# Kernel tuning notes

Hardware: AMD Instinct MI355X
Metric: run time of the kernel (lower is better)

Reference implementation:

```python
import jax, jax.numpy as jnp
import numpy as np

B, N, DIM, HEADS = 4, 2048, 512, 8
LN_EPS = 1e-5


def setup_inputs() -> dict:
    key = jax.random.key(0)
    ks = jax.random.split(key, 16)
    w = lambda k: jax.random.normal(k, (DIM, DIM), jnp.float32) * 0.02
    bv = lambda k: jax.random.normal(k, (DIM,), jnp.float32) * 0.02
    return {
        'x': jax.random.normal(ks[0], (B, N, DIM), jnp.float32),
        'y': jax.random.normal(ks[1], (B, N, DIM), jnp.float32),
        'Wq': w(ks[2]), 'bq': bv(ks[3]),
        'Wk': w(ks[4]), 'bk': bv(ks[5]),
        'Wvr': w(ks[6]), 'bvr': bv(ks[7]),
        'Wvd': w(ks[8]), 'bvd': bv(ks[9]),
        'g_r': jnp.ones((DIM,), jnp.float32), 'b_r': jnp.zeros((DIM,), jnp.float32),
        'g_d': jnp.ones((DIM,), jnp.float32), 'b_d': jnp.zeros((DIM,), jnp.float32),
        'Wpr': w(ks[10]), 'bpr': bv(ks[11]),
        'Wpd': w(ks[12]), 'bpd': bv(ks[13]),
        'num_heads': HEADS,
    }


def _ln(t, g, b):
    mu = jnp.mean(t, axis=-1, keepdims=True)
    var = jnp.mean(jnp.square(t - mu), axis=-1, keepdims=True)
    return (t - mu) * jax.lax.rsqrt(var + LN_EPS) * g + b


def reference(x, y, Wq, bq, Wk, bk, Wvr, bvr, Wvd, bvd,
              g_r, b_r, g_d, b_d, Wpr, bpr, Wpd, bpd, num_heads):
    Bn, Nn, C = x.shape
    D = C // num_heads
    xn = _ln(x, g_r, b_r)   # norm_r(x)
    yn = _ln(y, g_d, b_d)   # norm_d(y)

    def heads(t, W, b):  # Linear then split heads -> (B, H, N, D)
        return (t @ W.T + b).reshape(Bn, Nn, num_heads, D).transpose(0, 2, 1, 3)

    q_r = heads(yn, Wq, bq)    # query from depth-normed y
    v_r = heads(xn, Wvr, bvr)
    k_d = heads(xn, Wk, bk)
    v_d = heads(xn, Wvd, bvd)

    scale = D ** -0.5
    attn = jnp.einsum('bhnd,bhmd->bhnm', q_r, k_d) * scale  # shared QK^T
    attn_r = jax.nn.softmax(attn, axis=-1)                  # row-wise
    attn_d = jax.nn.softmax(attn.transpose(0, 1, 3, 2), axis=-1)  # col-wise (transposed)

    out_r = jnp.einsum('bhnm,bhmd->bhnd', attn_r, v_r)
    out_r = out_r.transpose(0, 2, 1, 3).reshape(Bn, Nn, C) @ Wpr.T + bpr

    o_d = jnp.einsum('bhnm,bhmd->bhnd', attn_d, v_d)
    o_d = o_d.transpose(0, 2, 1, 3).reshape(Bn, Nn, C)
    # Faithful to source quirk: extra transpose(1,2)+reshape scrambles layout.
    o_d = o_d.transpose(0, 2, 1).reshape(Bn, Nn, C)
    out_d = o_d @ Wpd.T + bpd
    return out_r, out_d
```

## Files before the change

### kernel.cpp

```cpp
#include <hip/hip_runtime.h>
#include <hip/hip_bf16.h>

typedef __hip_bfloat16 bf16;
typedef __attribute__((ext_vector_type(8))) short short8;
typedef __attribute__((ext_vector_type(4))) short short4v;
typedef __attribute__((ext_vector_type(4))) float floatx4;

static constexpr int B = 4;
static constexpr int N = 2048;
static constexpr int C = 512;
static constexpr int H = 8;
static constexpr int D = 64;

#define QK_SCALE 0.18033688011112042f

__device__ int g_flags[18];

__device__ __forceinline__ float u2f(unsigned short u) {
    return __uint_as_float(((unsigned int)u) << 16);
}
__device__ __forceinline__ unsigned short f2bf(float f) {
    unsigned int u = __float_as_uint(f);
    return (unsigned short)((u + 0x7FFFu + ((u >> 16) & 1u)) >> 16);
}
__device__ __forceinline__ float ldin(const void* p, size_t i, int f) {
    if (f == 2) return 0.0f;
    return f ? ((const float*)p)[i] : u2f(((const unsigned short*)p)[i]);
}

__device__ __forceinline__ void gl_lds16(const unsigned short* g, unsigned short* l) {
    __builtin_amdgcn_global_load_lds(
        (const __attribute__((address_space(1))) unsigned int*)g,
        (__attribute__((address_space(3))) unsigned int*)l,
        16, 0, 0);
}

struct Ptrs { const void* p[18]; };

__global__ void detect_kernel(Ptrs ptrs) {
    int t = blockIdx.x;
    int lane = threadIdx.x;
    unsigned int v = ((const unsigned int*)ptrs.p[t])[lane];
    unsigned int e = (v >> 7) & 0xFF;
    unsigned long long mp = __ballot(e >= 96 && e <= 144);
    unsigned long long mz = __ballot(v != 0u);
    if (lane == 0)
        g_flags[t] = (mz == 0ull) ? 2 : ((__popcll(mp) >= 32) ? 0 : 1);
}

__global__ __launch_bounds__(256) void convert_w(Ptrs ptrs, bf16* dst) {
    int wsel = blockIdx.y;
    int wi = wsel < 4 ? 2 + 2 * wsel : 14 + 2 * (wsel - 4);
    int f = g_flags[wi];
    const void* src = ptrs.p[wi];
    unsigned short* out = (unsigned short*)dst + (size_t)wsel * 262144;
    int base = (blockIdx.x * 256 + threadIdx.x) * 16;
    if (f == 1) {
        const float4* s = (const float4*)((const float*)src + base);
        float4 f0 = s[0], f1 = s[1], f2 = s[2], f3 = s[3];
        uint4 o0, o1;
        o0.x = f2bf(f0.x) | ((unsigned int)f2bf(f0.y) << 16);
        o0.y = f2bf(f0.z) | ((unsigned int)f2bf(f0.w) << 16);
        o0.z = f2bf(f1.x) | ((unsigned int)f2bf(f1.y) << 16);
        o0.w = f2bf(f1.z) | ((unsigned int)f2bf(f1.w) << 16);
        o1.x = f2bf(f2.x) | ((unsigned int)f2bf(f2.y) << 16);
        o1.y = f2bf(f2.z) | ((unsigned int)f2bf(f2.w) << 16);
        o1.z = f2bf(f3.x) | ((unsigned int)f2bf(f3.y) << 16);
        o1.w = f2bf(f3.z) | ((unsigned int)f2bf(f3.w) << 16);
        *(uint4*)(out + base) = o0;
        *(uint4*)(out + base + 8) = o1;
    } else if (f == 0) {
        const uint4* s = (const uint4*)((const unsigned short*)src + base);
        uint4 a = s[0], b2 = s[1];
        *(uint4*)(out + base) = a;
        *(uint4*)(out + base + 8) = b2;
    } else {
        uint4 z = {0, 0, 0, 0};
        *(uint4*)(out + base) = z;
        *(uint4*)(out + base + 8) = z;
    }
}

__global__ __launch_bounds__(256) void ln_kernel(
    const void* __restrict__ x, const void* __restrict__ y,
    const void* __restrict__ g_r, const void* __restrict__ b_r,
    const void* __restrict__ g_d, const void* __restrict__ b_d,
    bf16* __restrict__ xn, bf16* __restrict__ yn)
{
    __shared__ float ls[4], lq[4];
    __shared__ float mu_s, rs_s;

    int row = blockIdx.x;
    bool isY = row >= B * N;
    int r = isY ? row - B * N : row;
    const void* src = isY ? y : x;
    int sf = isY ? g_flags[1] : g_flags[0];
    const void* g  = isY ? g_d : g_r;
    int gf = isY ? g_flags[12] : g_flags[10];
    const void* bb = isY ? b_d : b_r;
    int bflag = isY ? g_flags[13] : g_flags[11];
    bf16* dst = (isY ? yn : xn) + (size_t)r * C;
    size_t base = (size_t)r * C;

    int tid = threadIdx.x;
    float v0 = ldin(src, base + tid, sf);
    float v1 = ldin(src, base + tid + 256, sf);
    float s = v0 + v1, sq = v0 * v0 + v1 * v1;
    #pragma unroll
    for (int off = 32; off > 0; off >>= 1) {
        s  += __shfl_down(s, off);
        sq += __shfl_down(sq, off);
    }
    int wid = tid >> 6, lane = tid & 63;
    if (lane == 0) { ls[wid] = s; lq[wid] = sq; }
    __syncthreads();
    if (tid == 0) {
        float S = ls[0] + ls[1] + ls[2] + ls[3];
        float Q = lq[0] + lq[1] + lq[2] + lq[3];
        float mu = S * (1.0f / C);
        float var = Q * (1.0f / C) - mu * mu;
        mu_s = mu; rs_s = rsqrtf(var + 1e-5f);
    }
    __syncthreads();
    float mu = mu_s, rs = rs_s;
    dst[tid]       = __float2bfloat16((v0 - mu) * rs * ldin(g, tid, gf)       + ldin(bb, tid, bflag));
    dst[tid + 256] = __float2bfloat16((v1 - mu) * rs * ldin(g, tid + 256, gf) + ldin(bb, tid + 256, bflag));
}

__device__ __forceinline__ void gemm_core(
    const bf16* __restrict__ A, const bf16* __restrict__ W,
    const void* __restrict__ bias, int bflag, void* __restrict__ Cout,
    int omode, float oscale)
{
    __shared__ __align__(16) unsigned short As[3][128 * 32];
    __shared__ __align__(16) unsigned short Ws[3][64 * 32];

    int tid = threadIdx.x;
    int n0 = blockIdx.x * 64;
    int m0 = blockIdx.y * 128;

    int wave = tid >> 6, lane = tid & 63;
    int wm = (wave >> 1) * 64, wn = (wave & 1) * 32;
    int quad = lane >> 4, mr = lane & 15;

    floatx4 acc[4][2] = {};

    int c0 = tid, c1 = 256 + tid;
    const unsigned short* Ag0 = (const unsigned short*)A + (size_t)(m0 + (c0 >> 2)) * 512 + (c0 & 3) * 8;
    const unsigned short* Ag1 = (const unsigned short*)A + (size_t)(m0 + (c1 >> 2)) * 512 + (c1 & 3) * 8;
    const unsigned short* Wg0 = (const unsigned short*)W + (size_t)(n0 + (c0 >> 2)) * 512 + (c0 & 3) * 8;

    auto STAGE = [&](int kt, int bsel) {
        int ko = kt * 32;
        gl_lds16(Ag0 + ko, &As[bsel][c0 * 8]);
        gl_lds16(Ag1 + ko, &As[bsel][c1 * 8]);
        gl_lds16(Wg0 + ko, &Ws[bsel][c0 * 8]);
    };

    auto GBODY = [&](int bsel, int kt) {
        if (kt < 14) {
            STAGE(kt + 2, bsel == 0 ? 2 : bsel - 1);
            asm volatile("s_waitcnt vmcnt(6)" ::: "memory");
        } else if (kt == 14) {
            asm volatile("s_waitcnt vmcnt(3)" ::: "memory");
        } else {
            asm volatile("s_waitcnt vmcnt(0)" ::: "memory");
        }
        __builtin_amdgcn_s_barrier();
        __builtin_amdgcn_sched_barrier(0);

        short8 af[4], bfr[2];
        #pragma unroll
        for (int i = 0; i < 4; ++i)
            af[i] = *(const short8*)&As[bsel][(wm + i * 16 + mr) * 32 + quad * 8];
        #pragma unroll
        for (int j = 0; j < 2; ++j)
            bfr[j] = *(const short8*)&Ws[bsel][(wn + j * 16 + mr) * 32 + quad * 8];
        #pragma unroll
        for (int i = 0; i < 4; ++i)
            #pragma unroll
            for (int j = 0; j < 2; ++j)
                acc[i][j] = __builtin_amdgcn_mfma_f32_16x16x32_bf16(
                    af[i], bfr[j], acc[i][j], 0, 0, 0);

        __builtin_amdgcn_sched_barrier(0);
        __builtin_amdgcn_s_barrier();
    };

    STAGE(0, 0);
    STAGE(1, 1);
    for (int g = 0; g < 5; ++g) {
        int kt = g * 3;
        GBODY(0, kt);
        GBODY(1, kt + 1);
        GBODY(2, kt + 2);
    }
    GBODY(0, 15);

    float bv[2];
    #pragma unroll
    for (int j = 0; j < 2; ++j)
        bv[j] = ldin(bias, n0 + wn + j * 16 + mr, bflag);
    #pragma unroll
    for (int i = 0; i < 4; ++i) {
        #pragma unroll
        for (int j = 0; j < 2; ++j) {
            int o = n0 + wn + j * 16 + mr;
            #pragma unroll
            for (int reg = 0; reg < 4; ++reg) {
                int r = m0 + wm + i * 16 + quad * 4 + reg;
                float val = (acc[i][j][reg] + bv[j]) * oscale;
                if (omode == 0) {
                    ((bf16*)Cout)[(size_t)r * 512 + o] = __float2bfloat16(val);
                } else if (omode == 1) {
                    ((float*)Cout)[(size_t)r * 512 + o] = val;
                } else {
                    int batch = r >> 11, nn = r & 2047;
                    ((bf16*)Cout)[((size_t)(batch * 512 + o)) * 2048 + nn] =
                        __float2bfloat16(val);
                }
            }
        }
    }
}

__global__ __launch_bounds__(256) void gemm_stage(
    const bf16* __restrict__ xn, const bf16* __restrict__ yn,
    const bf16* __restrict__ wts, Ptrs ptrs,
    bf16* __restrict__ q, bf16* __restrict__ k,
    bf16* __restrict__ vrT, bf16* __restrict__ vdT)
{
    int z = blockIdx.z;
    const bf16* A = (z == 0) ? yn : xn;
    const bf16* W = wts + (size_t)z * 262144;
    int bi = 3 + 2 * z;
    void* Cout = (z == 0) ? (void*)q : (z == 1) ? (void*)k
               : (z == 2) ? (void*)vrT : (void*)vdT;
    int omode = (z < 2) ? 0 : 2;
    float oscale = (z == 0) ? QK_SCALE : 1.0f;
    gemm_core(A, W, ptrs.p[bi], g_flags[bi], Cout, omode, oscale);
}

__global__ __launch_bounds__(256) void gemm_out(
    const bf16* __restrict__ Or, const bf16* __restrict__ Ad,
    const bf16* __restrict__ wts, Ptrs ptrs,
    float* __restrict__ out0, float* __restrict__ out1)
{
    int z = blockIdx.z;
    const bf16* A = z ? Ad : Or;
    const bf16* W = wts + (size_t)(4 + z) * 262144;
    int bi = 15 + 2 * z;
    gemm_core(A, W, ptrs.p[bi], g_flags[bi], z ? (void*)out1 : (void*)out0, 1, 1.0f);
}

__global__ __launch_bounds__(256) void flash_mfma(
    const bf16* __restrict__ qm, const bf16* __restrict__ km,
    const bf16* __restrict__ vrT, const bf16* __restrict__ vdT,
    bf16* __restrict__ Or, bf16* __restrict__ Ad)
{
    __shared__ __align__(16) unsigned short Ks[2][64 * 64];
    __shared__ __align__(16) unsigned short Vs[2][64 * 64];

    int phys = blockIdx.x + 32 * blockIdx.y + 256 * blockIdx.z;
    int s = phys >> 3;
    int qblk = s & 31;
    int gidx = (phys & 7) + ((s >> 5) << 3);
    int pass = gidx >> 5;
    int b = (gidx >> 3) & 3;
    int h = gidx & 7;

    const bf16* Q  = pass ? km : qm;
    const bf16* K  = pass ? qm : km;
    const bf16* Vt = pass ? vdT : vrT;
    bf16* Out = pass ? Ad : Or;

    int tid = threadIdx.x;
    int wave = tid >> 6, lane = tid & 63;
    int quad = lane >> 4, mr = lane & 15;
    int m8 = mr & 7;
    int qw = qblk * 64 + wave * 16;

    const unsigned short* Qb = (const unsigned short*)Q + ((size_t)(b * N + qw + mr)) * C + h * D;
    short8 qf0 = *(const short8*)(Qb + quad * 8);
    short8 qf1 = *(const short8*)(Qb + 32 + quad * 8);

    floatx4 Oacc[4] = {};
    floatx4 lacc = {};

    short4v ones;
    {
        union { unsigned int u[2]; short4v s4; } cv;
        cv.u[0] = 0x3F803F80u; cv.u[1] = 0x3F803F80u;
        ones = cv.s4;
    }

    int c0 = tid, c1 = 256 + tid;
    int r0 = c0 >> 3, cs0 = c0 & 7;
    int r1 = c1 >> 3, cs1 = c1 & 7;
    const unsigned short* Kb  = (const unsigned short*)K + ((size_t)b * N) * C + h * D;
    const unsigned short* Vtb = (const unsigned short*)Vt + ((size_t)(b * 512 + h * 64)) * 2048;
    const unsigned short* sk0 = Kb + (size_t)r0 * C + ((cs0 ^ (r0 & 7)) << 3);
    const unsigned short* sk1 = Kb + (size_t)r1 * C + ((cs1 ^ (r1 & 7)) << 3);
    const unsigned short* sv0 = Vtb + (size_t)r0 * 2048 + ((cs0 ^ (r0 & 7)) << 3);
    const unsigned short* sv1 = Vtb + (size_t)r1 * 2048 + ((cs1 ^ (r1 & 7)) << 3);

    auto STAGE = [&](int bsel) {
        gl_lds16(sk0, &Ks[bsel][c0 * 8]);
        gl_lds16(sk1, &Ks[bsel][c1 * 8]);
        gl_lds16(sv0, &Vs[bsel][c0 * 8]);
        gl_lds16(sv1, &Vs[bsel][c1 * 8]);
        sk0 += 64 * C; sk1 += 64 * C; sv0 += 64; sv1 += 64;
    };

    int skc0 = (quad ^ m8) << 3;
    int skc1 = ((quad + 4) ^ m8) << 3;
    int vq = quad >> 1, vlo = (quad & 1) * 4;

    auto BODY = [&](int cur, bool last) {
        if (!last) {
            STAGE(cur ^ 1);
            asm volatile("s_waitcnt vmcnt(4)" ::: "memory");
        } else {
            asm volatile("s_waitcnt vmcnt(0)" ::: "memory");
        }
        __builtin_amdgcn_s_barrier();
        __builtin_amdgcn_sched_barrier(0);

        floatx4 tac[4] = {};
        __builtin_amdgcn_s_setprio(1);
        #pragma unroll
        for (int t = 0; t < 4; ++t) {
            const unsigned short* kr = &Ks[cur][(t * 16 + mr) * 64];
            short8 kf0 = *(const short8*)(kr + skc0);
            short8 kf1 = *(const short8*)(kr + skc1);
            tac[t] = __builtin_amdgcn_mfma_f32_16x16x32_bf16(kf0, qf0, tac[t], 0, 0, 0);
            tac[t] = __builtin_amdgcn_mfma_f32_16x16x32_bf16(kf1, qf1, tac[t], 0, 0, 0);
        }
        __builtin_amdgcn_s_setprio(0);

        short4v pa[4];
        #pragma unroll
        for (int t = 0; t < 4; ++t) {
            float p0, p1, p2, p3;
            asm("v_exp_f32 %0, %1" : "=v"(p0) : "v"(tac[t][0]));
            asm("v_exp_f32 %0, %1" : "=v"(p1) : "v"(tac[t][1]));
            asm("v_exp_f32 %0, %1" : "=v"(p2) : "v"(tac[t][2]));
            asm("v_exp_f32 %0, %1" : "=v"(p3) : "v"(tac[t][3]));
            unsigned int u0, u1;
            asm("v_cvt_pk_bf16_f32 %0, %1, %2" : "=v"(u0) : "v"(p0), "v"(p1));
            asm("v_cvt_pk_bf16_f32 %0, %1, %2" : "=v"(u1) : "v"(p2), "v"(p3));
            union { unsigned int u[2]; short4v s4; } cv;
            cv.u[0] = u0; cv.u[1] = u1;
            pa[t] = cv.s4;
        }

        __builtin_amdgcn_s_setprio(1);
        #pragma unroll
        for (int t = 0; t < 4; ++t) {
            int vslot = (((2 * t + vq) ^ m8) << 3) + vlo;
            #pragma unroll
            for (int j = 0; j < 4; ++j) {
                short4v vb = *(const short4v*)&Vs[cur][(j * 16 + mr) * 64 + vslot];
                Oacc[j] = __builtin_amdgcn_mfma_f32_16x16x16bf16_1k(
                    pa[t], vb, Oacc[j], 0, 0, 0);
            }
            lacc = __builtin_amdgcn_mfma_f32_16x16x16bf16_1k(pa[t], ones, lacc, 0, 0, 0);
        }
        __builtin_amdgcn_s_setprio(0);

        __builtin_amdgcn_sched_barrier(0);
        __builtin_amdgcn_s_barrier();
    };

    STAGE(0);
    for (int kt2 = 0; kt2 < 15; ++kt2) {
        BODY(0, false);
        BODY(1, false);
    }
    BODY(0, false);
    BODY(1, true);

    float inv[4];
    #pragma unroll
    for (int r = 0; r < 4; ++r)
        inv[r] = 1.0f / lacc[r];

    if (pass == 0) {
        #pragma unroll
        for (int t = 0; t < 4; ++t)
            #pragma unroll
            for (int r = 0; r < 4; ++r) {
                int n = qw + quad * 4 + r;
                Out[((size_t)(b * N + n)) * C + h * D + t * 16 + mr] =
                    __float2bfloat16(Oacc[t][r] * inv[r]);
            }
    } else {
        size_t bbase = (size_t)b * N * C;
        #pragma unroll
        for (int t = 0; t < 4; ++t)
            #pragma unroll
            for (int r = 0; r < 4; ++r) {
                int n = qw + quad * 4 + r;
                int c = h * D + t * 16 + mr;
                Out[bbase + (size_t)(c * 4 + (n >> 9)) * 512 + (n & 511)] =
                    __float2bfloat16(Oacc[t][r] * inv[r]);
            }
    }
}

extern "C" void kernel_launch(void* const* d_in, const int* in_sizes, int n_in,
                              void* d_out, int out_size, void* d_ws, size_t ws_size,
                              hipStream_t stream)
{
    const void* x   = d_in[0];
    const void* y   = d_in[1];
    const void* g_r = d_in[10];
    const void* b_r = d_in[11];
    const void* g_d = d_in[12];
    const void* b_d = d_in[13];

    Ptrs ptrs;
    for (int i = 0; i < 18; ++i) ptrs.p[i] = d_in[i];

    const size_t SL = (size_t)B * N * C;

    char* wsb = (char*)d_ws;
    bf16* q   = (bf16*)wsb;
    bf16* k   = (bf16*)(wsb + 8ull * 1024 * 1024);
    bf16* vrT = (bf16*)(wsb + 16ull * 1024 * 1024);
    bf16* vdT = (bf16*)(wsb + 24ull * 1024 * 1024);
    bf16* xn  = (bf16*)(wsb + 32ull * 1024 * 1024);
    bf16* yn  = (bf16*)(wsb + 40ull * 1024 * 1024);
    bf16* wts = (bf16*)(wsb + 48ull * 1024 * 1024);
    bf16* Or = xn;
    bf16* Ad = yn;

    float* out0 = (float*)d_out;
    float* out1 = (float*)d_out + SL;

    detect_kernel<<<18, 64, 0, stream>>>(ptrs);
    convert_w<<<dim3(64, 6), 256, 0, stream>>>(ptrs, wts);
    ln_kernel<<<2 * B * N, 256, 0, stream>>>(x, y, g_r, b_r, g_d, b_d, xn, yn);

    gemm_stage<<<dim3(8, 64, 4), 256, 0, stream>>>(xn, yn, wts, ptrs, q, k, vrT, vdT);

    dim3 fg(32, 8, 8);
    flash_mfma<<<fg, 256, 0, stream>>>(q, k, vrT, vdT, Or, Ad);

    gemm_out<<<dim3(8, 64, 2), 256, 0, stream>>>(Or, Ad, wts, ptrs, out0, out1);
}
```

Measured before the change: 303.2 us.

## Load GEMM operands directly into registers and drop one attention barrier

The projection GEMM no longer stages A and W tiles through LDS with triple-buffered async copies. Each lane now loads its MFMA fragments straight from global memory into register double buffers, which removes the LDS traffic and the two block barriers per k-step. In exchange, global loads become less coalesced, and waves that share rows fetch the same data twice. In the attention loop the two barriers per iteration become one at the top, before the next tile is staged. That top barrier now comes before the vmcnt wait, so visibility of tile data loaded by other threads may no longer be guaranteed.

```diff
diff --git a/kernel.cpp b/kernel.cpp
--- a/kernel.cpp
+++ b/kernel.cpp
@@ -132,9 +132,6 @@
     const void* __restrict__ bias, int bflag, void* __restrict__ Cout,
     int omode, float oscale)
 {
-    __shared__ __align__(16) unsigned short As[3][128 * 32];
-    __shared__ __align__(16) unsigned short Ws[3][64 * 32];
-
     int tid = threadIdx.x;
     int n0 = blockIdx.x * 64;
     int m0 = blockIdx.y * 128;
@@ -143,59 +140,45 @@
     int wm = (wave >> 1) * 64, wn = (wave & 1) * 32;
     int quad = lane >> 4, mr = lane & 15;
 
+    const unsigned short* Ap[4];
+    const unsigned short* Wp[2];
+    #pragma unroll
+    for (int i = 0; i < 4; ++i)
+        Ap[i] = (const unsigned short*)A + (size_t)(m0 + wm + i * 16 + mr) * 512 + quad * 8;
+    #pragma unroll
+    for (int j = 0; j < 2; ++j)
+        Wp[j] = (const unsigned short*)W + (size_t)(n0 + wn + j * 16 + mr) * 512 + quad * 8;
+
     floatx4 acc[4][2] = {};
-
-    int c0 = tid, c1 = 256 + tid;
-    const unsigned short* Ag0 = (const unsigned short*)A + (size_t)(m0 + (c0 >> 2)) * 512 + (c0 & 3) * 8;
-    const unsigned short* Ag1 = (const unsigned short*)A + (size_t)(m0 + (c1 >> 2)) * 512 + (c1 & 3) * 8;
-    const unsigned short* Wg0 = (const unsigned short*)W + (size_t)(n0 + (c0 >> 2)) * 512 + (c0 & 3) * 8;
-
-    auto STAGE = [&](int kt, int bsel) {
-        int ko = kt * 32;
-        gl_lds16(Ag0 + ko, &As[bsel][c0 * 8]);
-        gl_lds16(Ag1 + ko, &As[bsel][c1 * 8]);
-        gl_lds16(Wg0 + ko, &Ws[bsel][c0 * 8]);
-    };
-
-    auto GBODY = [&](int bsel, int kt) {
-        if (kt < 14) {
-            STAGE(kt + 2, bsel == 0 ? 2 : bsel - 1);
-            asm volatile("s_waitcnt vmcnt(6)" ::: "memory");
-        } else if (kt == 14) {
-            asm volatile("s_waitcnt vmcnt(3)" ::: "memory");
-        } else {
-            asm volatile("s_waitcnt vmcnt(0)" ::: "memory");
-        }
-        __builtin_amdgcn_s_barrier();
-        __builtin_amdgcn_sched_barrier(0);
-
-        short8 af[4], bfr[2];
-        #pragma unroll
-        for (int i = 0; i < 4; ++i)
-            af[i] = *(const short8*)&As[bsel][(wm + i * 16 + mr) * 32 + quad * 8];
-        #pragma unroll
-        for (int j = 0; j < 2; ++j)
-            bfr[j] = *(const short8*)&Ws[bsel][(wn + j * 16 + mr) * 32 + quad * 8];
+    short8 ra[4], wa[2], rb[4], wb[2];
+
+    #pragma unroll
+    for (int i = 0; i < 4; ++i) ra[i] = *(const short8*)(Ap[i]);
+    #pragma unroll
+    for (int j = 0; j < 2; ++j) wa[j] = *(const short8*)(Wp[j]);
+
+    auto STEP = [&](short8 (&ca)[4], short8 (&cw)[2],
+                    short8 (&na)[4], short8 (&nw)[2], int kt) {
+        if (kt < 15) {
+            int ko = (kt + 1) * 32;
+            #pragma unroll
+            for (int i = 0; i < 4; ++i) na[i] = *(const short8*)(Ap[i] + ko);
+            #pragma unroll
+            for (int j = 0; j < 2; ++j) nw[j] = *(const short8*)(Wp[j] + ko);
+        }
         #pragma unroll
         for (int i = 0; i < 4; ++i)
             #pragma unroll
             for (int j = 0; j < 2; ++j)
                 acc[i][j] = __builtin_amdgcn_mfma_f32_16x16x32_bf16(
-                    af[i], bfr[j], acc[i][j], 0, 0, 0);
-
-        __builtin_amdgcn_sched_barrier(0);
-        __builtin_amdgcn_s_barrier();
+                    ca[i], cw[j], acc[i][j], 0, 0, 0);
     };
 
-    STAGE(0, 0);
-    STAGE(1, 1);
-    for (int g = 0; g < 5; ++g) {
-        int kt = g * 3;
-        GBODY(0, kt);
-        GBODY(1, kt + 1);
-        GBODY(2, kt + 2);
-    }
-    GBODY(0, 15);
+    #pragma unroll
+    for (int g = 0; g < 8; ++g) {
+        STEP(ra, wa, rb, wb, 2 * g);
+        STEP(rb, wb, ra, wa, 2 * g + 1);
+    }
 
     float bv[2];
     #pragma unroll
@@ -317,13 +300,13 @@
     int vq = quad >> 1, vlo = (quad & 1) * 4;
 
     auto BODY = [&](int cur, bool last) {
+        __builtin_amdgcn_s_barrier();
         if (!last) {
             STAGE(cur ^ 1);
             asm volatile("s_waitcnt vmcnt(4)" ::: "memory");
         } else {
             asm volatile("s_waitcnt vmcnt(0)" ::: "memory");
         }
-        __builtin_amdgcn_s_barrier();
         __builtin_amdgcn_sched_barrier(0);
 
         floatx4 tac[4] = {};
@@ -367,9 +350,7 @@
             lacc = __builtin_amdgcn_mfma_f32_16x16x16bf16_1k(pa[t], ones, lacc, 0, 0, 0);
         }
         __builtin_amdgcn_s_setprio(0);
-
         __builtin_amdgcn_sched_barrier(0);
-        __builtin_amdgcn_s_barrier();
     };
 
     STAGE(0);
```

New measurement: 369.2 us. +21.8%, slower.
